# Kernel optimization log

Hardware: AMD Instinct MI355X
Metric: run time of the kernel (lower is better)

The kernel has to match this reference:

```python
import jax, jax.numpy as jnp
import numpy as np


def setup_inputs() -> dict:
    key = jax.random.key(0)
    k1, k2, k3 = jax.random.split(key, 3)
    B, C, H, W = 4, 32, 320, 320
    NC = 21  # num_category
    return {
        "input_F": jax.random.normal(k1, (B, C, H, W), dtype=jnp.float32),
        "input_logit": jax.random.normal(k2, (B, NC, H, W), dtype=jnp.float32),
        "weight": jnp.asarray(1.0, dtype=jnp.float32),
        "compatibility": jax.random.normal(k3, (NC, NC, 1, 1), dtype=jnp.float32) * 0.1,
        "bias": jnp.zeros((NC,), dtype=jnp.float32),
        "kernel_len": 7,
    }


def _local_crf_pass(input_F, Q, weight, kernel_len):
    # Fused local_diff + exp-kernel + local_crf aggregation.
    # For each of the k*k neighborhood offsets (zero padding):
    #   diff[b,h,w]  = sum_c (F[b,c,h,w] - F_shift[b,c,h,w])^2 / C
    #   kern[b,h,w]  = weight * exp(-diff)
    #   out[b,q,h,w] += kern * Q_shift[b,q,h,w]
    B, C, H, W = input_F.shape
    pad = kernel_len // 2
    Fp = jnp.pad(input_F, ((0, 0), (0, 0), (pad, pad), (pad, pad)))
    Qp = jnp.pad(Q, ((0, 0), (0, 0), (pad, pad), (pad, pad)))
    out = jnp.zeros_like(Q)
    inv_c = jnp.float32(1.0 / C)
    for di in range(kernel_len):
        for dj in range(kernel_len):
            Fs = Fp[:, :, di:di + H, dj:dj + W]
            diff = jnp.sum((input_F - Fs) ** 2, axis=1) * inv_c  # [B,H,W]
            kern = weight * jnp.exp(-diff)
            out = out + kern[:, None, :, :] * Qp[:, :, di:di + H, dj:dj + W]
    return out / jnp.float32(kernel_len)


def reference(input_F, input_logit, weight, compatibility, bias, kernel_len):
    Q = jax.nn.softmax(input_logit, axis=1)  # softmax over categories
    out = _local_crf_pass(input_F, Q, weight, kernel_len)  # [B,NC,H,W]
    # 1x1 conv with sigmoid(compatibility) + bias
    compat = jax.nn.sigmoid(compatibility[:, :, 0, 0])  # [NC_out, NC_in]
    out = jnp.einsum('oi,bihw->bohw', compat, out) + bias[None, :, None, None]
    return input_logit - out
```

## Files before the change

### kernel.cpp

```cpp
#include <hip/hip_runtime.h>

#define Bn 4
#define Cn 32
#define Hn 320
#define Wn 320
#define NCn 21
#define HWSZ (Hn*Wn)

#define THr 32
#define TWr 64
#define HHr 38
#define HWIDr 70
#define FWr 72
#define NG 8
#define QSTRr 76

typedef _Float16 h2 __attribute__((ext_vector_type(2)));

#define LDS_F   (NG*HHr*FWr*4)
#define LDS_Q   (NCn*HHr*QSTRr)
#define LDS_TOTAL (LDS_F + LDS_Q)

__device__ __forceinline__ h2 fp8pair_lo(uint32_t w) {
  uint32_t t = ((w & 0x000000FFu) << 8) | ((w & 0x0000FF00u) << 16);
  uint32_t r = (t & 0x80008000u) | ((t >> 1) & 0x3FFF3FFFu);
  return __builtin_bit_cast(h2, r);
}
__device__ __forceinline__ h2 fp8pair_hi(uint32_t w) {
  uint32_t t = ((w >> 8) & 0x0000FF00u) | (w & 0xFF000000u);
  uint32_t r = (t & 0x80008000u) | ((t >> 1) & 0x3FFF3FFFu);
  return __builtin_bit_cast(h2, r);
}

__device__ __forceinline__ float fdot2f(h2 a, h2 b, float c) {
#if __has_builtin(__builtin_amdgcn_fdot2)
  return __builtin_amdgcn_fdot2(a, b, c, false);
#else
  return c + (float)a[0]*(float)b[0] + (float)a[1]*(float)b[1];
#endif
}

__global__ __attribute__((amdgpu_flat_work_group_size(512, 512),
                          amdgpu_waves_per_eu(2, 2)))
void crf_fused2(
    const float* __restrict__ Fin, const float* __restrict__ logit,
    const float* __restrict__ weight, const float* __restrict__ compat,
    const float* __restrict__ bias, float* __restrict__ out)
{
  extern __shared__ char smem[];
  uint32_t* fbuf = (uint32_t*)smem;
  uint8_t*  qbuf = (uint8_t*)(smem + LDS_F);

  const int bid = blockIdx.x;
  const int b   = bid / 50;
  const int r   = bid % 50;
  const int th  = r / 5, twi = r % 5;
  const int h0  = th * THr, w0 = twi * TWr;
  const int tid = threadIdx.x;

  const float* fb0 = Fin + (size_t)b * Cn * HWSZ;
  for (int idx = tid; idx < NG * HHr * FWr; idx += 512) {
    int lw = idx % FWr;
    int r2 = idx / FWr;
    int lh = r2 % HHr;
    int g  = r2 / HHr;
    int gh = h0 - 3 + lh, gw = w0 - 3 + lw;
    uint32_t wd = 0u;
    if (lw < HWIDr && (unsigned)gh < (unsigned)Hn && (unsigned)gw < (unsigned)Wn) {
      const float* p = fb0 + (size_t)(4 * g) * HWSZ + gh * Wn + gw;
      float f0 = p[0], f1 = p[HWSZ], f2 = p[2 * HWSZ], f3 = p[3 * HWSZ];
      int pk = __builtin_amdgcn_cvt_pk_fp8_f32(f0, f1, 0, false);
      pk = __builtin_amdgcn_cvt_pk_fp8_f32(f2, f3, pk, true);
      wd = (uint32_t)pk;
    }
    fbuf[idx] = wd;
  }

  const float* lg0 = logit + (size_t)b * NCn * HWSZ;
  for (int p = tid; p < HHr * HWIDr; p += 512) {
    int lw = p % HWIDr, lh = p / HWIDr;
    int gh = h0 - 3 + lh, gw = w0 - 3 + lw;
    uint8_t* qp = qbuf + lh * QSTRr + lw;
    if ((unsigned)gh < (unsigned)Hn && (unsigned)gw < (unsigned)Wn) {
      const float* lp = lg0 + gh * Wn + gw;
      float v[NCn];
      float m = -1e30f;
      #pragma unroll
      for (int o = 0; o < NCn; o++) { v[o] = lp[(size_t)o * HWSZ]; m = fmaxf(m, v[o]); }
      float s = 0.f;
      #pragma unroll
      for (int o = 0; o < NCn; o++) { v[o] = __expf(v[o] - m); s += v[o]; }
      float inv = 1.0f / s;
      #pragma unroll
      for (int o = 0; o < NCn; o++) {
        int pk = __builtin_amdgcn_cvt_pk_fp8_f32(v[o] * inv, 0.f, 0, false);
        qp[(size_t)o * HHr * QSTRr] = (uint8_t)(pk & 0xff);
      }
    } else {
      #pragma unroll
      for (int o = 0; o < NCn; o++) qp[(size_t)o * HHr * QSTRr] = 0;
    }
  }
  __syncthreads();

  const int ty = tid >> 4;
  const int tg = tid & 15;
  const int x  = tg << 2;

  h2 cen[NG][8];
  #pragma unroll
  for (int g = 0; g < NG; g++) {
    const uint32_t* fc = fbuf + (g * HHr + (ty + 3)) * FWr + (x + 3);
    #pragma unroll
    for (int p = 0; p < 4; p++) {
      uint32_t w = fc[p];
      cen[g][2 * p]     = fp8pair_lo(w);
      cen[g][2 * p + 1] = fp8pair_hi(w);
    }
  }

  float acc[4][NCn];
  #pragma unroll
  for (int p = 0; p < 4; p++)
    #pragma unroll
    for (int o = 0; o < NCn; o++) acc[p][o] = 0.f;

  #pragma unroll 1
  for (int di = 0; di < 7; di++) {
    const int lhn = ty + di;
    float ds[4][7];
    #pragma unroll
    for (int p = 0; p < 4; p++)
      #pragma unroll
      for (int j = 0; j < 7; j++) ds[p][j] = 0.f;

    #pragma unroll
    for (int g = 0; g < NG; g++) {
      const uint32_t* frow = fbuf + (g * HHr + lhn) * FWr + x;
      uint4 n0 = *(const uint4*)(frow);
      uint4 n1 = *(const uint4*)(frow + 4);
      uint4 n2 = *(const uint4*)(frow + 8);
      uint32_t nw[10] = {n0.x, n0.y, n0.z, n0.w, n1.x, n1.y, n1.z, n1.w, n2.x, n2.y};
      #pragma unroll
      for (int k = 0; k < 10; k++) {
        h2 lo = fp8pair_lo(nw[k]);
        h2 hi = fp8pair_hi(nw[k]);
        #pragma unroll
        for (int p = 0; p < 4; p++) {
          const int j = k - p;
          if (j >= 0 && j < 7) {
            h2 d0 = cen[g][2 * p] - lo;
            h2 d1 = cen[g][2 * p + 1] - hi;
            float t = fdot2f(d0, d0, ds[p][j]);
            ds[p][j] = fdot2f(d1, d1, t);
          }
        }
      }
    }

    #pragma unroll
    for (int p = 0; p < 4; p++)
      #pragma unroll
      for (int j = 0; j < 7; j++)
        ds[p][j] = __expf(ds[p][j] * -2048.0f);

    #pragma unroll
    for (int o = 0; o < NCn; o++) {
      const uint32_t* qrow = (const uint32_t*)(qbuf + (o * HHr + lhn) * QSTRr + x);
      uint32_t q0 = qrow[0], q1 = qrow[1], q2 = qrow[2];
      float qv[10];
      qv[0] = __builtin_amdgcn_cvt_f32_fp8((int)q0, 0);
      qv[1] = __builtin_amdgcn_cvt_f32_fp8((int)q0, 1);
      qv[2] = __builtin_amdgcn_cvt_f32_fp8((int)q0, 2);
      qv[3] = __builtin_amdgcn_cvt_f32_fp8((int)q0, 3);
      qv[4] = __builtin_amdgcn_cvt_f32_fp8((int)q1, 0);
      qv[5] = __builtin_amdgcn_cvt_f32_fp8((int)q1, 1);
      qv[6] = __builtin_amdgcn_cvt_f32_fp8((int)q1, 2);
      qv[7] = __builtin_amdgcn_cvt_f32_fp8((int)q1, 3);
      qv[8] = __builtin_amdgcn_cvt_f32_fp8((int)q2, 0);
      qv[9] = __builtin_amdgcn_cvt_f32_fp8((int)q2, 1);
      #pragma unroll
      for (int p = 0; p < 4; p++)
        #pragma unroll
        for (int j = 0; j < 7; j++)
          acc[p][o] = fmaf(ds[p][j], qv[p + j], acc[p][o]);
    }
  }

  __syncthreads();
  float* cmat = (float*)(smem + LDS_F);
  {
    float wgt = weight[0] * (1.0f / 7.0f);
    for (int i = tid; i < NCn * NCn; i += 512) {
      float c = compat[i];
      cmat[i] = wgt / (1.f + __expf(-c));
    }
  }
  __syncthreads();

  const int gh = h0 + ty;
  const size_t pixoff = (size_t)b * NCn * HWSZ + (size_t)gh * Wn + (w0 + x);
  const float* lc = logit + pixoff;
  float* oc = out + pixoff;
  #pragma unroll
  for (int o = 0; o < NCn; o++) {
    float s0 = 0.f, s1 = 0.f, s2 = 0.f, s3 = 0.f;
    #pragma unroll
    for (int i2 = 0; i2 < NCn; i2++) {
      float cm = cmat[o * NCn + i2];
      s0 = fmaf(cm, acc[0][i2], s0);
      s1 = fmaf(cm, acc[1][i2], s1);
      s2 = fmaf(cm, acc[2][i2], s2);
      s3 = fmaf(cm, acc[3][i2], s3);
    }
    float bo = bias[o];
    const float4 lg = *(const float4*)(lc + (size_t)o * HWSZ);
    float4 rr;
    rr.x = lg.x - s0 - bo;
    rr.y = lg.y - s1 - bo;
    rr.z = lg.z - s2 - bo;
    rr.w = lg.w - s3 - bo;
    *(float4*)(oc + (size_t)o * HWSZ) = rr;
  }
}

extern "C" void kernel_launch(void* const* d_in, const int* in_sizes, int n_in,
                              void* d_out, int out_size, void* d_ws, size_t ws_size,
                              hipStream_t stream) {
  (void)in_sizes; (void)n_in; (void)out_size; (void)d_ws; (void)ws_size;
  const float* F      = (const float*)d_in[0];
  const float* logit  = (const float*)d_in[1];
  const float* weight = (const float*)d_in[2];
  const float* compat = (const float*)d_in[3];
  const float* bias   = (const float*)d_in[4];
  float* out = (float*)d_out;

  hipFuncSetAttribute((const void*)crf_fused2,
                      hipFuncAttributeMaxDynamicSharedMemorySize, LDS_TOTAL);
  crf_fused2<<<dim3(Bn * 50), dim3(512), LDS_TOTAL, stream>>>(
      F, logit, weight, compat, bias, out);
}
```

Before: 253.4 us.

## Shrink tiles to 16x32 with 2 pixels per thread and 256-thread blocks

Cuts the spatial tile from 32x64 to 16x32, uses 256-thread blocks with 2 output pixels per thread instead of 4, and launches 800 blocks instead of 200. The neighbour loads become uint2 reads, and the Q bytes are realigned with a 64-bit shift. The aim is to fix poor GPU fill (200 blocks across 256 CUs) and to lower register pressure so more waves fit. The trade is a larger halo overhead: more redundant F and softmax staging per output pixel, plus less register reuse of neighbour data.

```diff
diff --git a/kernel.cpp b/kernel.cpp
--- a/kernel.cpp
+++ b/kernel.cpp
@@ -7,18 +7,18 @@
 #define NCn 21
 #define HWSZ (Hn*Wn)
 
-#define THr 32
-#define TWr 64
-#define HHr 38
-#define HWIDr 70
-#define FWr 72
+#define TH 16
+#define TW 32
+#define HH 22
+#define HCOL 38
+#define FW 40
 #define NG 8
-#define QSTRr 76
+#define QSTR 40
 
 typedef _Float16 h2 __attribute__((ext_vector_type(2)));
 
-#define LDS_F   (NG*HHr*FWr*4)
-#define LDS_Q   (NCn*HHr*QSTRr)
+#define LDS_F   (NG*HH*FW*4)
+#define LDS_Q   (NCn*HH*QSTR)
 #define LDS_TOTAL (LDS_F + LDS_Q)
 
 __device__ __forceinline__ h2 fp8pair_lo(uint32_t w) {
@@ -40,9 +40,7 @@
 #endif
 }
 
-__global__ __attribute__((amdgpu_flat_work_group_size(512, 512),
-                          amdgpu_waves_per_eu(2, 2)))
-void crf_fused2(
+__global__ __launch_bounds__(256, 3) void crf_fused3(
     const float* __restrict__ Fin, const float* __restrict__ logit,
     const float* __restrict__ weight, const float* __restrict__ compat,
     const float* __restrict__ bias, float* __restrict__ out)
@@ -52,21 +50,21 @@
   uint8_t*  qbuf = (uint8_t*)(smem + LDS_F);
 
   const int bid = blockIdx.x;
-  const int b   = bid / 50;
-  const int r   = bid % 50;
-  const int th  = r / 5, twi = r % 5;
-  const int h0  = th * THr, w0 = twi * TWr;
+  const int b   = bid / 200;
+  const int r   = bid % 200;
+  const int th  = r / 10, twi = r % 10;
+  const int h0  = th * TH, w0 = twi * TW;
   const int tid = threadIdx.x;
 
   const float* fb0 = Fin + (size_t)b * Cn * HWSZ;
-  for (int idx = tid; idx < NG * HHr * FWr; idx += 512) {
-    int lw = idx % FWr;
-    int r2 = idx / FWr;
-    int lh = r2 % HHr;
-    int g  = r2 / HHr;
+  for (int idx = tid; idx < NG * HH * FW; idx += 256) {
+    int lw = idx % FW;
+    int r2 = idx / FW;
+    int lh = r2 % HH;
+    int g  = r2 / HH;
     int gh = h0 - 3 + lh, gw = w0 - 3 + lw;
     uint32_t wd = 0u;
-    if (lw < HWIDr && (unsigned)gh < (unsigned)Hn && (unsigned)gw < (unsigned)Wn) {
+    if (lw < HCOL && (unsigned)gh < (unsigned)Hn && (unsigned)gw < (unsigned)Wn) {
       const float* p = fb0 + (size_t)(4 * g) * HWSZ + gh * Wn + gw;
       float f0 = p[0], f1 = p[HWSZ], f2 = p[2 * HWSZ], f3 = p[3 * HWSZ];
       int pk = __builtin_amdgcn_cvt_pk_fp8_f32(f0, f1, 0, false);
@@ -77,10 +75,10 @@
   }
 
   const float* lg0 = logit + (size_t)b * NCn * HWSZ;
-  for (int p = tid; p < HHr * HWIDr; p += 512) {
-    int lw = p % HWIDr, lh = p / HWIDr;
+  for (int p = tid; p < HH * HCOL; p += 256) {
+    int lw = p % HCOL, lh = p / HCOL;
     int gh = h0 - 3 + lh, gw = w0 - 3 + lw;
-    uint8_t* qp = qbuf + lh * QSTRr + lw;
+    uint8_t* qp = qbuf + lh * QSTR + lw;
     if ((unsigned)gh < (unsigned)Hn && (unsigned)gw < (unsigned)Wn) {
       const float* lp = lg0 + gh * Wn + gw;
       float v[NCn];
@@ -94,93 +92,92 @@
       #pragma unroll
       for (int o = 0; o < NCn; o++) {
         int pk = __builtin_amdgcn_cvt_pk_fp8_f32(v[o] * inv, 0.f, 0, false);
-        qp[(size_t)o * HHr * QSTRr] = (uint8_t)(pk & 0xff);
+        qp[(size_t)o * HH * QSTR] = (uint8_t)(pk & 0xff);
       }
     } else {
       #pragma unroll
-      for (int o = 0; o < NCn; o++) qp[(size_t)o * HHr * QSTRr] = 0;
+      for (int o = 0; o < NCn; o++) qp[(size_t)o * HH * QSTR] = 0;
     }
   }
   __syncthreads();
 
   const int ty = tid >> 4;
   const int tg = tid & 15;
-  const int x  = tg << 2;
-
-  h2 cen[NG][8];
+  const int x2 = tg << 1;
+
+  h2 cen[NG][4];
   #pragma unroll
   for (int g = 0; g < NG; g++) {
-    const uint32_t* fc = fbuf + (g * HHr + (ty + 3)) * FWr + (x + 3);
-    #pragma unroll
-    for (int p = 0; p < 4; p++) {
+    const uint32_t* fc = fbuf + (g * HH + (ty + 3)) * FW + (x2 + 3);
+    #pragma unroll
+    for (int p = 0; p < 2; p++) {
       uint32_t w = fc[p];
       cen[g][2 * p]     = fp8pair_lo(w);
       cen[g][2 * p + 1] = fp8pair_hi(w);
     }
   }
 
-  float acc[4][NCn];
+  float acc[2][NCn];
   #pragma unroll
-  for (int p = 0; p < 4; p++)
+  for (int p = 0; p < 2; p++)
     #pragma unroll
     for (int o = 0; o < NCn; o++) acc[p][o] = 0.f;
+
+  const int qw0 = x2 >> 2;
+  const int qsh = (x2 & 3) * 8;
 
   #pragma unroll 1
   for (int di = 0; di < 7; di++) {
     const int lhn = ty + di;
-    float ds[4][7];
-    #pragma unroll
-    for (int p = 0; p < 4; p++)
+    float ds[2][7];
+    #pragma unroll
+    for (int p = 0; p < 2; p++)
       #pragma unroll
       for (int j = 0; j < 7; j++) ds[p][j] = 0.f;
 
     #pragma unroll
     for (int g = 0; g < NG; g++) {
-      const uint32_t* frow = fbuf + (g * HHr + lhn) * FWr + x;
-      uint4 n0 = *(const uint4*)(frow);
-      uint4 n1 = *(const uint4*)(frow + 4);
-      uint4 n2 = *(const uint4*)(frow + 8);
-      uint32_t nw[10] = {n0.x, n0.y, n0.z, n0.w, n1.x, n1.y, n1.z, n1.w, n2.x, n2.y};
-      #pragma unroll
-      for (int k = 0; k < 10; k++) {
-        h2 lo = fp8pair_lo(nw[k]);
-        h2 hi = fp8pair_hi(nw[k]);
+      const uint2* frow = (const uint2*)(fbuf + (g * HH + lhn) * FW + x2);
+      uint2 a = frow[0], bb = frow[1], c = frow[2], d = frow[3];
+      uint32_t nw[8] = {a.x, a.y, bb.x, bb.y, c.x, c.y, d.x, d.y};
+      h2 nlo[8], nhi[8];
+      #pragma unroll
+      for (int k = 0; k < 8; k++) { nlo[k] = fp8pair_lo(nw[k]); nhi[k] = fp8pair_hi(nw[k]); }
+      #pragma unroll
+      for (int p = 0; p < 2; p++) {
         #pragma unroll
-        for (int p = 0; p < 4; p++) {
-          const int j = k - p;
-          if (j >= 0 && j < 7) {
-            h2 d0 = cen[g][2 * p] - lo;
-            h2 d1 = cen[g][2 * p + 1] - hi;
-            float t = fdot2f(d0, d0, ds[p][j]);
-            ds[p][j] = fdot2f(d1, d1, t);
-          }
+        for (int j = 0; j < 7; j++) {
+          h2 d0 = cen[g][2 * p]     - nlo[p + j];
+          h2 d1 = cen[g][2 * p + 1] - nhi[p + j];
+          float t = fdot2f(d0, d0, ds[p][j]);
+          ds[p][j] = fdot2f(d1, d1, t);
         }
       }
     }
 
     #pragma unroll
-    for (int p = 0; p < 4; p++)
+    for (int p = 0; p < 2; p++)
       #pragma unroll
       for (int j = 0; j < 7; j++)
         ds[p][j] = __expf(ds[p][j] * -2048.0f);
 
     #pragma unroll
     for (int o = 0; o < NCn; o++) {
-      const uint32_t* qrow = (const uint32_t*)(qbuf + (o * HHr + lhn) * QSTRr + x);
+      const uint32_t* qrow = (const uint32_t*)(qbuf + (o * HH + lhn) * QSTR) + qw0;
       uint32_t q0 = qrow[0], q1 = qrow[1], q2 = qrow[2];
-      float qv[10];
-      qv[0] = __builtin_amdgcn_cvt_f32_fp8((int)q0, 0);
-      qv[1] = __builtin_amdgcn_cvt_f32_fp8((int)q0, 1);
-      qv[2] = __builtin_amdgcn_cvt_f32_fp8((int)q0, 2);
-      qv[3] = __builtin_amdgcn_cvt_f32_fp8((int)q0, 3);
-      qv[4] = __builtin_amdgcn_cvt_f32_fp8((int)q1, 0);
-      qv[5] = __builtin_amdgcn_cvt_f32_fp8((int)q1, 1);
-      qv[6] = __builtin_amdgcn_cvt_f32_fp8((int)q1, 2);
-      qv[7] = __builtin_amdgcn_cvt_f32_fp8((int)q1, 3);
-      qv[8] = __builtin_amdgcn_cvt_f32_fp8((int)q2, 0);
-      qv[9] = __builtin_amdgcn_cvt_f32_fp8((int)q2, 1);
-      #pragma unroll
-      for (int p = 0; p < 4; p++)
+      uint32_t a0 = (uint32_t)(((((uint64_t)q1 << 32) | q0)) >> qsh);
+      uint32_t a1 = (uint32_t)(((((uint64_t)q2 << 32) | q1)) >> qsh);
+      float qv[8];
+      qv[0] = __builtin_amdgcn_cvt_f32_fp8((int)a0, 0);
+      qv[1] = __builtin_amdgcn_cvt_f32_fp8((int)a0, 1);
+      qv[2] = __builtin_amdgcn_cvt_f32_fp8((int)a0, 2);
+      qv[3] = __builtin_amdgcn_cvt_f32_fp8((int)a0, 3);
+      qv[4] = __builtin_amdgcn_cvt_f32_fp8((int)a1, 0);
+      qv[5] = __builtin_amdgcn_cvt_f32_fp8((int)a1, 1);
+      qv[6] = __builtin_amdgcn_cvt_f32_fp8((int)a1, 2);
+      qv[7] = __builtin_amdgcn_cvt_f32_fp8((int)a1, 3);
+      #pragma unroll
+      for (int p = 0; p < 2; p++)
         #pragma unroll
         for (int j = 0; j < 7; j++)
           acc[p][o] = fmaf(ds[p][j], qv[p + j], acc[p][o]);
@@ -188,10 +185,10 @@
   }
 
   __syncthreads();
-  float* cmat = (float*)(smem + LDS_F);
+  float* cmat = (float*)smem;
   {
     float wgt = weight[0] * (1.0f / 7.0f);
-    for (int i = tid; i < NCn * NCn; i += 512) {
+    for (int i = tid; i < NCn * NCn; i += 256) {
       float c = compat[i];
       cmat[i] = wgt / (1.f + __expf(-c));
     }
@@ -199,28 +196,24 @@
   __syncthreads();
 
   const int gh = h0 + ty;
-  const size_t pixoff = (size_t)b * NCn * HWSZ + (size_t)gh * Wn + (w0 + x);
+  const size_t pixoff = (size_t)b * NCn * HWSZ + (size_t)gh * Wn + (w0 + x2);
   const float* lc = logit + pixoff;
   float* oc = out + pixoff;
   #pragma unroll
   for (int o = 0; o < NCn; o++) {
-    float s0 = 0.f, s1 = 0.f, s2 = 0.f, s3 = 0.f;
+    float s0 = 0.f, s1 = 0.f;
     #pragma unroll
     for (int i2 = 0; i2 < NCn; i2++) {
       float cm = cmat[o * NCn + i2];
       s0 = fmaf(cm, acc[0][i2], s0);
       s1 = fmaf(cm, acc[1][i2], s1);
-      s2 = fmaf(cm, acc[2][i2], s2);
-      s3 = fmaf(cm, acc[3][i2], s3);
     }
     float bo = bias[o];
-    const float4 lg = *(const float4*)(lc + (size_t)o * HWSZ);
-    float4 rr;
+    const float2 lg = *(const float2*)(lc + (size_t)o * HWSZ);
+    float2 rr;
     rr.x = lg.x - s0 - bo;
     rr.y = lg.y - s1 - bo;
-    rr.z = lg.z - s2 - bo;
-    rr.w = lg.w - s3 - bo;
-    *(float4*)(oc + (size_t)o * HWSZ) = rr;
+    *(float2*)(oc + (size_t)o * HWSZ) = rr;
   }
 }
 
@@ -235,8 +228,8 @@
   const float* bias   = (const float*)d_in[4];
   float* out = (float*)d_out;
 
-  hipFuncSetAttribute((const void*)crf_fused2,
+  hipFuncSetAttribute((const void*)crf_fused3,
                       hipFuncAttributeMaxDynamicSharedMemorySize, LDS_TOTAL);
-  crf_fused2<<<dim3(Bn * 50), dim3(512), LDS_TOTAL, stream>>>(
+  crf_fused3<<<dim3(Bn * 200), dim3(256), LDS_TOTAL, stream>>>(
       F, logit, weight, compat, bias, out);
 }
```

New measurement: 265.6 us. +4.8%, slower.
